# Kernel optimization log

Hardware: AMD Instinct MI355X
Metric: run time of the kernel (lower is better)

## Reference

```python
import jax, jax.numpy as jnp
import numpy as np

D = 1024  # input_size == hidden_size (required by the module's math)
B = 32768

def _linear_params(key, out_dim, in_dim):
    kw, kb = jax.random.split(key)
    bound = 1.0 / np.sqrt(in_dim)
    W = jax.random.uniform(kw, (out_dim, in_dim), jnp.float32, -bound, bound)
    b = jax.random.uniform(kb, (out_dim,), jnp.float32, -bound, bound)
    return W, b

def setup_inputs() -> dict:
    key = jax.random.key(0)
    ks = jax.random.split(key, 8)
    inp = {
        "input": jax.random.normal(ks[0], (B, D), jnp.float32),
        "hidden": jax.random.normal(ks[1], (B, D), jnp.float32),
    }
    names = ["ir", "hr", "iz", "hz", "in_", "hn"]
    for name, k in zip(names, ks[2:]):
        W, b = _linear_params(k, D, D)
        inp[f"W_{name}"] = W
        inp[f"b_{name}"] = b
    return inp

def reference(input, hidden, W_ir, b_ir, W_hr, b_hr, W_iz, b_iz, W_hz, b_hz, W_in_, b_in_, W_hn, b_hn):
    # Fuse the three input-side projections and three hidden-side projections
    # into two GEMMs each mathematically identical to six separate Linears.
    lin = lambda x, W, b: x @ W.T + b
    r_t = jax.nn.sigmoid(lin(input, W_ir, b_ir) + lin(hidden, W_hr, b_hr))
    z_t = jax.nn.sigmoid(lin(input, W_iz, b_iz) + lin(hidden, W_hz, b_hz))
    n_t = jnp.tanh(lin(input, W_in_, b_in_) + r_t * lin(hidden, W_hn, b_hn))
    h_t = (1.0 - z_t) * n_t + z_t * hidden
    return (h_t, h_t)
```

## Files before the change

kernel.cpp:

```cpp
#include <hip/hip_runtime.h>
#include <stdint.h>

#define DD 1024
#define BATCH 32768

typedef unsigned short u16;
typedef __attribute__((ext_vector_type(8))) __bf16 bf16x8;
typedef __attribute__((ext_vector_type(4))) float f32x4;
typedef __attribute__((ext_vector_type(4))) unsigned int u32x4;

__device__ __forceinline__ u16 f2bf(float x) {
  unsigned int u = __builtin_bit_cast(unsigned int, x);
  u = u + 0x7FFFu + ((u >> 16) & 1u);
  return (u16)(u >> 16);
}

__global__ void cvt_f32_to_bf16(const float4* __restrict__ src,
                                ushort4* __restrict__ dst, int n4) {
  int i = blockIdx.x * blockDim.x + threadIdx.x;
  int stride = gridDim.x * blockDim.x;
  for (; i < n4; i += stride) {
    float4 v = src[i];
    ushort4 o;
    o.x = f2bf(v.x); o.y = f2bf(v.y); o.z = f2bf(v.z); o.w = f2bf(v.w);
    dst[i] = o;
  }
}

#define A_IN_U 0
#define A_H_U  8192
#define W_U(g) (16384 + (g) * 4096)

__device__ __forceinline__ bf16x8 ld8(const u16* p) {
  u32x4 v = *reinterpret_cast<const u32x4*>(p);
  return __builtin_bit_cast(bf16x8, v);
}

__device__ __forceinline__ f32x4 mfma16(bf16x8 a, bf16x8 b, f32x4 c) {
  return __builtin_amdgcn_mfma_f32_16x16x32_bf16(a, b, c, 0, 0, 0);
}

__device__ __forceinline__ void stage_chunk(const u16* grow, u16* ldsdst) {
  int l = threadIdx.x & 63;
  int r = l >> 3;
  int s = l & 7;
  const u16* src = grow + r * DD + ((s ^ r) << 3);
  __builtin_amdgcn_global_load_lds(
      (const __attribute__((address_space(1))) void*)src,
      (__attribute__((address_space(3))) void*)ldsdst, 16, 0, 0);
}

__global__ __launch_bounds__(256, 2) void gru_fused(
    const u16* __restrict__ ain, const u16* __restrict__ ah,
    const u16* __restrict__ wall, const float* __restrict__ hidf,
    const float* __restrict__ b_ir, const float* __restrict__ b_hr,
    const float* __restrict__ b_iz, const float* __restrict__ b_hz,
    const float* __restrict__ b_in, const float* __restrict__ b_hn,
    float* __restrict__ out) {
  __shared__ __align__(16) u16 lds[40960];

  int bid = blockIdx.x;
  int wg = ((bid & 7) << 9) | (bid >> 3);
  int nb = wg >> 8;
  int mb = wg & 255;

  int tid = threadIdx.x;
  int wid = tid >> 6;
  int lane = tid & 63;
  int r15 = lane & 15;
  int kb = lane >> 4;
  int wm = wid >> 1;
  int wn = wid & 1;

  const f32x4 zero = {0.f, 0.f, 0.f, 0.f};
  f32x4 acc_r[4][2], acc_z[4][2], acc_n[4][2], acc_hn[4][2];
#pragma unroll
  for (int i = 0; i < 4; ++i)
#pragma unroll
    for (int j = 0; j < 2; ++j) {
      acc_r[i][j] = zero; acc_z[i][j] = zero;
      acc_n[i][j] = zero; acc_hn[i][j] = zero;
    }

  const u16* ain_t = ain + ((size_t)(mb * 128) << 10);
  const u16* ah_t  = ah  + ((size_t)(mb * 128) << 10);
  const u16* w_t   = wall + ((size_t)(nb * 64) << 10);

  for (int kt = 0; kt < 16; ++kt) {
    int kcol = kt << 6;
    __syncthreads();
#pragma unroll
    for (int j = 0; j < 4; ++j) {
      int c = (j << 2) | wid;
      stage_chunk(ain_t + ((size_t)c << 13) + kcol, &lds[A_IN_U + c * 512]);
      stage_chunk(ah_t  + ((size_t)c << 13) + kcol, &lds[A_H_U  + c * 512]);
    }
#pragma unroll
    for (int g = 0; g < 6; ++g) {
      const u16* wg_t = w_t + ((size_t)g << 20) + kcol;
#pragma unroll
      for (int j = 0; j < 2; ++j) {
        int c = (j << 2) | wid;
        stage_chunk(wg_t + ((size_t)c << 13), &lds[W_U(g) + c * 512]);
      }
    }
    __syncthreads();

#pragma unroll
    for (int ks = 0; ks < 2; ++ks) {
      bf16x8 afi[4], afh[4];
#pragma unroll
      for (int i = 0; i < 4; ++i) {
        int Rm = (wm << 6) + (i << 4) + r15;
        int sl = ((ks << 2) | kb) ^ (Rm & 7);
        afi[i] = ld8(&lds[A_IN_U + Rm * 64 + sl * 8]);
        afh[i] = ld8(&lds[A_H_U  + Rm * 64 + sl * 8]);
      }
#pragma unroll
      for (int jf = 0; jf < 2; ++jf) {
        int Rn = (wn << 5) + (jf << 4) + r15;
        int sl = ((ks << 2) | kb) ^ (Rn & 7);
        bf16x8 bir = ld8(&lds[W_U(0) + Rn * 64 + sl * 8]);
        bf16x8 bhr = ld8(&lds[W_U(1) + Rn * 64 + sl * 8]);
        bf16x8 biz = ld8(&lds[W_U(2) + Rn * 64 + sl * 8]);
        bf16x8 bhz = ld8(&lds[W_U(3) + Rn * 64 + sl * 8]);
        bf16x8 bin = ld8(&lds[W_U(4) + Rn * 64 + sl * 8]);
        bf16x8 bhn = ld8(&lds[W_U(5) + Rn * 64 + sl * 8]);
#pragma unroll
        for (int i = 0; i < 4; ++i) {
          acc_r[i][jf]  = mfma16(afi[i], bir, acc_r[i][jf]);
          acc_r[i][jf]  = mfma16(afh[i], bhr, acc_r[i][jf]);
          acc_z[i][jf]  = mfma16(afi[i], biz, acc_z[i][jf]);
          acc_z[i][jf]  = mfma16(afh[i], bhz, acc_z[i][jf]);
          acc_n[i][jf]  = mfma16(afi[i], bin, acc_n[i][jf]);
          acc_hn[i][jf] = mfma16(afh[i], bhn, acc_hn[i][jf]);
        }
      }
    }
  }

#pragma unroll
  for (int jf = 0; jf < 2; ++jf) {
    int col = (nb << 6) + (wn << 5) + (jf << 4) + r15;
    float brc = b_ir[col] + b_hr[col];
    float bzc = b_iz[col] + b_hz[col];
    float bnc = b_in[col];
    float bhc = b_hn[col];
#pragma unroll
    for (int i = 0; i < 4; ++i) {
      int row0 = (mb << 7) + (wm << 6) + (i << 4) + (kb << 2);
#pragma unroll
      for (int q = 0; q < 4; ++q) {
        int row = row0 + q;
        float vr = acc_r[i][jf][q] + brc;
        float vz = acc_z[i][jf][q] + bzc;
        float vn = acc_n[i][jf][q] + bnc;
        float vh = acc_hn[i][jf][q] + bhc;
        float rg = __builtin_amdgcn_rcpf(1.f + __expf(-vr));
        float zg = __builtin_amdgcn_rcpf(1.f + __expf(-vz));
        float pre = vn + rg * vh;
        float ax = fabsf(pre);
        float e2 = __expf(-2.f * ax);
        float th = copysignf((1.f - e2) * __builtin_amdgcn_rcpf(1.f + e2), pre);
        float hp = hidf[((size_t)row << 10) + col];
        float h = (1.f - zg) * th + zg * hp;
        size_t o = ((size_t)row << 10) + col;
        out[o] = h;
        out[o + (size_t)BATCH * DD] = h;
      }
    }
  }
}

extern "C" void kernel_launch(void* const* d_in, const int* in_sizes, int n_in,
                              void* d_out, int out_size, void* d_ws, size_t ws_size,
                              hipStream_t stream) {
  (void)in_sizes; (void)n_in; (void)out_size; (void)ws_size;
  const float* inp = (const float*)d_in[0];
  const float* hid = (const float*)d_in[1];
  u16* ws_in  = (u16*)d_ws;
  u16* ws_hid = ws_in + (size_t)BATCH * DD;
  u16* ws_w   = ws_hid + (size_t)BATCH * DD;

  int n4a = BATCH * DD / 4;
  hipLaunchKernelGGL(cvt_f32_to_bf16, dim3(4096), dim3(256), 0, stream,
                     (const float4*)inp, (ushort4*)ws_in, n4a);
  hipLaunchKernelGGL(cvt_f32_to_bf16, dim3(4096), dim3(256), 0, stream,
                     (const float4*)hid, (ushort4*)ws_hid, n4a);
  for (int g = 0; g < 6; ++g) {
    hipLaunchKernelGGL(cvt_f32_to_bf16, dim3(512), dim3(256), 0, stream,
                       (const float4*)d_in[2 + 2 * g],
                       (ushort4*)(ws_w + (size_t)g * DD * DD), DD * DD / 4);
  }
  hipLaunchKernelGGL(gru_fused, dim3(4096), dim3(256), 0, stream,
                     ws_in, ws_hid, ws_w, hid,
                     (const float*)d_in[3], (const float*)d_in[5],
                     (const float*)d_in[7], (const float*)d_in[9],
                     (const float*)d_in[11], (const float*)d_in[13],
                     (float*)d_out);
}
```

Measured before the change: 549.0 us.

## Double-buffer GRU GEMM staging, enlarge tile to 256 rows, fuse conversion kernels

The eight per-tensor fp32-to-bf16 conversion launches are merged into one kernel with a fixed block-to-tensor mapping. The fused GEMM now uses 512-thread blocks covering 256 rows by 64 columns. The K step drops to 32, and a double-buffered LDS pipeline prefetches the next K slice while computing the current one, using raw barriers, vmcnt waits and s_setprio around the MFMA block. This aims to hide global-load latency and halve weight-tile reloads per row, at the cost of more LDS per block and hand-tuned waitcnt logic that must match the issued load counts.

```diff
diff --git a/kernel.cpp b/kernel.cpp
--- a/kernel.cpp
+++ b/kernel.cpp
@@ -15,21 +15,33 @@
   return (u16)(u >> 16);
 }
 
-__global__ void cvt_f32_to_bf16(const float4* __restrict__ src,
-                                ushort4* __restrict__ dst, int n4) {
-  int i = blockIdx.x * blockDim.x + threadIdx.x;
-  int stride = gridDim.x * blockDim.x;
-  for (; i < n4; i += stride) {
-    float4 v = src[i];
+__global__ void cvt_all(const float4* __restrict__ in0, const float4* __restrict__ in1,
+                        const float4* __restrict__ w0, const float4* __restrict__ w1,
+                        const float4* __restrict__ w2, const float4* __restrict__ w3,
+                        const float4* __restrict__ w4, const float4* __restrict__ w5,
+                        ushort4* __restrict__ o0, ushort4* __restrict__ o1,
+                        ushort4* __restrict__ ow) {
+  int b = blockIdx.x;
+  const float4* s; ushort4* d; int rel;
+  if (b < 2048)      { s = in0; d = o0; rel = b; }
+  else if (b < 4096) { s = in1; d = o1; rel = b - 2048; }
+  else {
+    int t = b - 4096; int g = t >> 6; rel = t & 63;
+    s = (g == 0) ? w0 : (g == 1) ? w1 : (g == 2) ? w2 : (g == 3) ? w3 : (g == 4) ? w4 : w5;
+    d = ow + (size_t)g * 262144;
+  }
+  int i0 = rel * 4096 + threadIdx.x;
+#pragma unroll
+  for (int j = 0; j < 16; ++j) {
+    int i = i0 + j * 256;
+    float4 v = s[i];
     ushort4 o;
     o.x = f2bf(v.x); o.y = f2bf(v.y); o.z = f2bf(v.z); o.w = f2bf(v.w);
-    dst[i] = o;
-  }
-}
-
-#define A_IN_U 0
-#define A_H_U  8192
-#define W_U(g) (16384 + (g) * 4096)
+    d[i] = o;
+  }
+}
+
+#define BUF_U 28672
 
 __device__ __forceinline__ bf16x8 ld8(const u16* p) {
   u32x4 v = *reinterpret_cast<const u32x4*>(p);
@@ -40,29 +52,25 @@
   return __builtin_amdgcn_mfma_f32_16x16x32_bf16(a, b, c, 0, 0, 0);
 }
 
-__device__ __forceinline__ void stage_chunk(const u16* grow, u16* ldsdst) {
-  int l = threadIdx.x & 63;
-  int r = l >> 3;
-  int s = l & 7;
-  const u16* src = grow + r * DD + ((s ^ r) << 3);
+__device__ __forceinline__ void stage_one(const u16* src, const u16* dst) {
   __builtin_amdgcn_global_load_lds(
       (const __attribute__((address_space(1))) void*)src,
-      (__attribute__((address_space(3))) void*)ldsdst, 16, 0, 0);
-}
-
-__global__ __launch_bounds__(256, 2) void gru_fused(
+      (__attribute__((address_space(3))) void*)dst, 16, 0, 0);
+}
+
+__global__ __launch_bounds__(512, 2) void gru_fused(
     const u16* __restrict__ ain, const u16* __restrict__ ah,
     const u16* __restrict__ wall, const float* __restrict__ hidf,
     const float* __restrict__ b_ir, const float* __restrict__ b_hr,
     const float* __restrict__ b_iz, const float* __restrict__ b_hz,
     const float* __restrict__ b_in, const float* __restrict__ b_hn,
     float* __restrict__ out) {
-  __shared__ __align__(16) u16 lds[40960];
+  __shared__ __align__(16) u16 lds[2 * BUF_U];
 
   int bid = blockIdx.x;
-  int wg = ((bid & 7) << 9) | (bid >> 3);
-  int nb = wg >> 8;
-  int mb = wg & 255;
+  int wg = ((bid & 7) << 8) | (bid >> 3);
+  int nb = wg >> 7;
+  int mb = wg & 127;
 
   int tid = threadIdx.x;
   int wid = tid >> 6;
@@ -82,61 +90,74 @@
       acc_n[i][j] = zero; acc_hn[i][j] = zero;
     }
 
-  const u16* ain_t = ain + ((size_t)(mb * 128) << 10);
-  const u16* ah_t  = ah  + ((size_t)(mb * 128) << 10);
-  const u16* w_t   = wall + ((size_t)(nb * 64) << 10);
-
-  for (int kt = 0; kt < 16; ++kt) {
-    int kcol = kt << 6;
-    __syncthreads();
-#pragma unroll
-    for (int j = 0; j < 4; ++j) {
-      int c = (j << 2) | wid;
-      stage_chunk(ain_t + ((size_t)c << 13) + kcol, &lds[A_IN_U + c * 512]);
-      stage_chunk(ah_t  + ((size_t)c << 13) + kcol, &lds[A_H_U  + c * 512]);
-    }
-#pragma unroll
-    for (int g = 0; g < 6; ++g) {
-      const u16* wg_t = w_t + ((size_t)g << 20) + kcol;
-#pragma unroll
-      for (int j = 0; j < 2; ++j) {
-        int c = (j << 2) | wid;
-        stage_chunk(wg_t + ((size_t)c << 13), &lds[W_U(g) + c * 512]);
+  int lrow = lane >> 2;
+  unsigned koff = (unsigned)(((lane & 3) ^ (lrow & 3)) << 3);
+  const u16* ain_r = ain + (unsigned)(mb * 256 + lrow) * DD + koff;
+  const u16* ah_r  = ah  + (unsigned)(mb * 256 + lrow) * DD + koff;
+  const u16* w_r   = wall + (unsigned)(nb * 64 + lrow) * DD + koff;
+  int sub = wid & 3;
+  int g0 = wid >> 2;
+  const u16* wsrc = w_r + (unsigned)(sub * 16) * DD;
+
+  auto stage = [&](int kt, int bufb) {
+    unsigned kc = (unsigned)(kt << 5);
+    stage_one(ain_r + (unsigned)(wid * 16) * DD + kc,       &lds[bufb + wid * 512]);
+    stage_one(ain_r + (unsigned)((wid + 8) * 16) * DD + kc, &lds[bufb + (wid + 8) * 512]);
+    stage_one(ah_r  + (unsigned)(wid * 16) * DD + kc,       &lds[bufb + 8192 + wid * 512]);
+    stage_one(ah_r  + (unsigned)((wid + 8) * 16) * DD + kc, &lds[bufb + 8192 + (wid + 8) * 512]);
+    stage_one(wsrc + ((unsigned)g0 << 20) + kc,        &lds[bufb + 16384 + g0 * 2048 + sub * 512]);
+    stage_one(wsrc + ((unsigned)(g0 + 2) << 20) + kc,  &lds[bufb + 16384 + (g0 + 2) * 2048 + sub * 512]);
+    stage_one(wsrc + ((unsigned)(g0 + 4) << 20) + kc,  &lds[bufb + 16384 + (g0 + 4) * 2048 + sub * 512]);
+  };
+
+  auto compute = [&](int bufb) {
+    const u16* B = &lds[bufb];
+    bf16x8 afi[4], afh[4];
+#pragma unroll
+    for (int i = 0; i < 4; ++i) {
+      int Rm = (wm << 6) + (i << 4) + r15;
+      int sl = kb ^ (Rm & 3);
+      afi[i] = ld8(B + Rm * 32 + sl * 8);
+      afh[i] = ld8(B + 8192 + Rm * 32 + sl * 8);
+    }
+    __builtin_amdgcn_s_setprio(1);
+#pragma unroll
+    for (int jf = 0; jf < 2; ++jf) {
+      int Rn = (wn << 5) + (jf << 4) + r15;
+      int sl = kb ^ (Rn & 3);
+      const u16* W0 = B + 16384 + Rn * 32 + sl * 8;
+      bf16x8 bir = ld8(W0);
+      bf16x8 bhr = ld8(W0 + 2048);
+      bf16x8 biz = ld8(W0 + 4096);
+      bf16x8 bhz = ld8(W0 + 6144);
+      bf16x8 bin = ld8(W0 + 8192);
+      bf16x8 bhn = ld8(W0 + 10240);
+#pragma unroll
+      for (int i = 0; i < 4; ++i) {
+        acc_r[i][jf]  = mfma16(afi[i], bir, acc_r[i][jf]);
+        acc_r[i][jf]  = mfma16(afh[i], bhr, acc_r[i][jf]);
+        acc_z[i][jf]  = mfma16(afi[i], biz, acc_z[i][jf]);
+        acc_z[i][jf]  = mfma16(afh[i], bhz, acc_z[i][jf]);
+        acc_n[i][jf]  = mfma16(afi[i], bin, acc_n[i][jf]);
+        acc_hn[i][jf] = mfma16(afh[i], bhn, acc_hn[i][jf]);
       }
     }
-    __syncthreads();
-
-#pragma unroll
-    for (int ks = 0; ks < 2; ++ks) {
-      bf16x8 afi[4], afh[4];
-#pragma unroll
-      for (int i = 0; i < 4; ++i) {
-        int Rm = (wm << 6) + (i << 4) + r15;
-        int sl = ((ks << 2) | kb) ^ (Rm & 7);
-        afi[i] = ld8(&lds[A_IN_U + Rm * 64 + sl * 8]);
-        afh[i] = ld8(&lds[A_H_U  + Rm * 64 + sl * 8]);
-      }
-#pragma unroll
-      for (int jf = 0; jf < 2; ++jf) {
-        int Rn = (wn << 5) + (jf << 4) + r15;
-        int sl = ((ks << 2) | kb) ^ (Rn & 7);
-        bf16x8 bir = ld8(&lds[W_U(0) + Rn * 64 + sl * 8]);
-        bf16x8 bhr = ld8(&lds[W_U(1) + Rn * 64 + sl * 8]);
-        bf16x8 biz = ld8(&lds[W_U(2) + Rn * 64 + sl * 8]);
-        bf16x8 bhz = ld8(&lds[W_U(3) + Rn * 64 + sl * 8]);
-        bf16x8 bin = ld8(&lds[W_U(4) + Rn * 64 + sl * 8]);
-        bf16x8 bhn = ld8(&lds[W_U(5) + Rn * 64 + sl * 8]);
-#pragma unroll
-        for (int i = 0; i < 4; ++i) {
-          acc_r[i][jf]  = mfma16(afi[i], bir, acc_r[i][jf]);
-          acc_r[i][jf]  = mfma16(afh[i], bhr, acc_r[i][jf]);
-          acc_z[i][jf]  = mfma16(afi[i], biz, acc_z[i][jf]);
-          acc_z[i][jf]  = mfma16(afh[i], bhz, acc_z[i][jf]);
-          acc_n[i][jf]  = mfma16(afi[i], bin, acc_n[i][jf]);
-          acc_hn[i][jf] = mfma16(afh[i], bhn, acc_hn[i][jf]);
-        }
-      }
-    }
+    __builtin_amdgcn_s_setprio(0);
+  };
+
+  stage(0, 0);
+  for (int kt = 0; kt < 32; ++kt) {
+    if (kt < 31) {
+      stage(kt + 1, ((kt + 1) & 1) * BUF_U);
+      asm volatile("s_waitcnt vmcnt(7)" ::: "memory");
+    } else {
+      asm volatile("s_waitcnt vmcnt(0)" ::: "memory");
+    }
+    __builtin_amdgcn_s_barrier();
+    __builtin_amdgcn_sched_barrier(0);
+    compute((kt & 1) * BUF_U);
+    asm volatile("s_waitcnt lgkmcnt(0)" ::: "memory");
+    __builtin_amdgcn_s_barrier();
   }
 
 #pragma unroll
@@ -148,7 +169,7 @@
     float bhc = b_hn[col];
 #pragma unroll
     for (int i = 0; i < 4; ++i) {
-      int row0 = (mb << 7) + (wm << 6) + (i << 4) + (kb << 2);
+      int row0 = (mb << 8) + (wm << 6) + (i << 4) + (kb << 2);
 #pragma unroll
       for (int q = 0; q < 4; ++q) {
         int row = row0 + q;
@@ -182,17 +203,14 @@
   u16* ws_hid = ws_in + (size_t)BATCH * DD;
   u16* ws_w   = ws_hid + (size_t)BATCH * DD;
 
-  int n4a = BATCH * DD / 4;
-  hipLaunchKernelGGL(cvt_f32_to_bf16, dim3(4096), dim3(256), 0, stream,
-                     (const float4*)inp, (ushort4*)ws_in, n4a);
-  hipLaunchKernelGGL(cvt_f32_to_bf16, dim3(4096), dim3(256), 0, stream,
-                     (const float4*)hid, (ushort4*)ws_hid, n4a);
-  for (int g = 0; g < 6; ++g) {
-    hipLaunchKernelGGL(cvt_f32_to_bf16, dim3(512), dim3(256), 0, stream,
-                       (const float4*)d_in[2 + 2 * g],
-                       (ushort4*)(ws_w + (size_t)g * DD * DD), DD * DD / 4);
-  }
-  hipLaunchKernelGGL(gru_fused, dim3(4096), dim3(256), 0, stream,
+  hipLaunchKernelGGL(cvt_all, dim3(4480), dim3(256), 0, stream,
+                     (const float4*)inp, (const float4*)hid,
+                     (const float4*)d_in[2], (const float4*)d_in[4],
+                     (const float4*)d_in[6], (const float4*)d_in[8],
+                     (const float4*)d_in[10], (const float4*)d_in[12],
+                     (ushort4*)ws_in, (ushort4*)ws_hid, (ushort4*)ws_w);
+
+  hipLaunchKernelGGL(gru_fused, dim3(2048), dim3(512), 0, stream,
                      ws_in, ws_hid, ws_w, hid,
                      (const float*)d_in[3], (const float*)d_in[5],
                      (const float*)d_in[7], (const float*)d_in[9],
```

New measurement: 672.1 us. 22.4% more time.

## Switch GRU GEMM to 32x32x16 MFMA, merge conversions, remap block order

Applied to the files above, without the earlier changes.

Replaces the 16x16x32 bf16 MFMA tiles with 32x32x16 tiles, so each wave issues fewer, larger MFMAs and does fewer LDS fragment reads per unit of work. The epilogue is rewritten to match the 32x32 accumulator layout. The eight separate f32-to-bf16 conversion launches are merged into one kernel with a fixed per-block work split. The block-to-tile mapping is also changed so that consecutive blocks in an XCD group walk the N tiles of one M stripe, which is meant to improve L2 reuse of the activation rows. These changes risk different register pressure and LDS bank-conflict patterns.

```diff
diff --git a/kernel.cpp b/kernel.cpp
--- a/kernel.cpp
+++ b/kernel.cpp
@@ -6,7 +6,7 @@
 
 typedef unsigned short u16;
 typedef __attribute__((ext_vector_type(8))) __bf16 bf16x8;
-typedef __attribute__((ext_vector_type(4))) float f32x4;
+typedef __attribute__((ext_vector_type(16))) float f32x16;
 typedef __attribute__((ext_vector_type(4))) unsigned int u32x4;
 
 __device__ __forceinline__ u16 f2bf(float x) {
@@ -15,15 +15,29 @@
   return (u16)(u >> 16);
 }
 
-__global__ void cvt_f32_to_bf16(const float4* __restrict__ src,
-                                ushort4* __restrict__ dst, int n4) {
-  int i = blockIdx.x * blockDim.x + threadIdx.x;
-  int stride = gridDim.x * blockDim.x;
-  for (; i < n4; i += stride) {
-    float4 v = src[i];
+__global__ void cvt_all(const float4* __restrict__ in0, const float4* __restrict__ in1,
+                        const float4* __restrict__ w0, const float4* __restrict__ w1,
+                        const float4* __restrict__ w2, const float4* __restrict__ w3,
+                        const float4* __restrict__ w4, const float4* __restrict__ w5,
+                        ushort4* __restrict__ o0, ushort4* __restrict__ o1,
+                        ushort4* __restrict__ ow) {
+  int b = blockIdx.x;
+  const float4* s; ushort4* d; int rel;
+  if (b < 2048)      { s = in0; d = o0; rel = b; }
+  else if (b < 4096) { s = in1; d = o1; rel = b - 2048; }
+  else {
+    int t = b - 4096; int g = t >> 6; rel = t & 63;
+    s = (g == 0) ? w0 : (g == 1) ? w1 : (g == 2) ? w2 : (g == 3) ? w3 : (g == 4) ? w4 : w5;
+    d = ow + (size_t)g * 262144;
+  }
+  int i0 = rel * 4096 + threadIdx.x;
+#pragma unroll
+  for (int j = 0; j < 16; ++j) {
+    int i = i0 + j * 256;
+    float4 v = s[i];
     ushort4 o;
     o.x = f2bf(v.x); o.y = f2bf(v.y); o.z = f2bf(v.z); o.w = f2bf(v.w);
-    dst[i] = o;
+    d[i] = o;
   }
 }
 
@@ -36,8 +50,8 @@
   return __builtin_bit_cast(bf16x8, v);
 }
 
-__device__ __forceinline__ f32x4 mfma16(bf16x8 a, bf16x8 b, f32x4 c) {
-  return __builtin_amdgcn_mfma_f32_16x16x32_bf16(a, b, c, 0, 0, 0);
+__device__ __forceinline__ f32x16 mfma32(bf16x8 a, bf16x8 b, f32x16 c) {
+  return __builtin_amdgcn_mfma_f32_32x32x16_bf16(a, b, c, 0, 0, 0);
 }
 
 __device__ __forceinline__ void stage_chunk(const u16* grow, u16* ldsdst) {
@@ -60,31 +74,31 @@
   __shared__ __align__(16) u16 lds[40960];
 
   int bid = blockIdx.x;
-  int wg = ((bid & 7) << 9) | (bid >> 3);
-  int nb = wg >> 8;
-  int mb = wg & 255;
+  int x = bid & 7;
+  int s = bid >> 3;
+  int mb = (x << 5) | (s >> 4);
+  int nb = s & 15;
 
   int tid = threadIdx.x;
   int wid = tid >> 6;
   int lane = tid & 63;
-  int r15 = lane & 15;
-  int kb = lane >> 4;
+  int c31 = lane & 31;
+  int khalf = lane >> 5;
   int wm = wid >> 1;
   int wn = wid & 1;
 
-  const f32x4 zero = {0.f, 0.f, 0.f, 0.f};
-  f32x4 acc_r[4][2], acc_z[4][2], acc_n[4][2], acc_hn[4][2];
-#pragma unroll
-  for (int i = 0; i < 4; ++i)
-#pragma unroll
-    for (int j = 0; j < 2; ++j) {
-      acc_r[i][j] = zero; acc_z[i][j] = zero;
-      acc_n[i][j] = zero; acc_hn[i][j] = zero;
-    }
+  f32x16 acc_r[2], acc_z[2], acc_n[2], acc_hn[2];
+#pragma unroll
+  for (int i = 0; i < 2; ++i) {
+    acc_r[i] = (f32x16)0.f; acc_z[i] = (f32x16)0.f;
+    acc_n[i] = (f32x16)0.f; acc_hn[i] = (f32x16)0.f;
+  }
 
   const u16* ain_t = ain + ((size_t)(mb * 128) << 10);
   const u16* ah_t  = ah  + ((size_t)(mb * 128) << 10);
   const u16* w_t   = wall + ((size_t)(nb * 64) << 10);
+
+  int possw = c31 & 7;
 
   for (int kt = 0; kt < 16; ++kt) {
     int kcol = kt << 6;
@@ -107,67 +121,61 @@
     __syncthreads();
 
 #pragma unroll
-    for (int ks = 0; ks < 2; ++ks) {
-      bf16x8 afi[4], afh[4];
-#pragma unroll
-      for (int i = 0; i < 4; ++i) {
-        int Rm = (wm << 6) + (i << 4) + r15;
-        int sl = ((ks << 2) | kb) ^ (Rm & 7);
-        afi[i] = ld8(&lds[A_IN_U + Rm * 64 + sl * 8]);
-        afh[i] = ld8(&lds[A_H_U  + Rm * 64 + sl * 8]);
+    for (int ks = 0; ks < 4; ++ks) {
+      int pos = (((ks << 1) | khalf) ^ possw) << 3;
+      bf16x8 afi[2], afh[2];
+#pragma unroll
+      for (int i = 0; i < 2; ++i) {
+        int Rm = (wm << 6) + (i << 5) + c31;
+        afi[i] = ld8(&lds[A_IN_U + Rm * 64 + pos]);
+        afh[i] = ld8(&lds[A_H_U  + Rm * 64 + pos]);
       }
-#pragma unroll
-      for (int jf = 0; jf < 2; ++jf) {
-        int Rn = (wn << 5) + (jf << 4) + r15;
-        int sl = ((ks << 2) | kb) ^ (Rn & 7);
-        bf16x8 bir = ld8(&lds[W_U(0) + Rn * 64 + sl * 8]);
-        bf16x8 bhr = ld8(&lds[W_U(1) + Rn * 64 + sl * 8]);
-        bf16x8 biz = ld8(&lds[W_U(2) + Rn * 64 + sl * 8]);
-        bf16x8 bhz = ld8(&lds[W_U(3) + Rn * 64 + sl * 8]);
-        bf16x8 bin = ld8(&lds[W_U(4) + Rn * 64 + sl * 8]);
-        bf16x8 bhn = ld8(&lds[W_U(5) + Rn * 64 + sl * 8]);
-#pragma unroll
-        for (int i = 0; i < 4; ++i) {
-          acc_r[i][jf]  = mfma16(afi[i], bir, acc_r[i][jf]);
-          acc_r[i][jf]  = mfma16(afh[i], bhr, acc_r[i][jf]);
-          acc_z[i][jf]  = mfma16(afi[i], biz, acc_z[i][jf]);
-          acc_z[i][jf]  = mfma16(afh[i], bhz, acc_z[i][jf]);
-          acc_n[i][jf]  = mfma16(afi[i], bin, acc_n[i][jf]);
-          acc_hn[i][jf] = mfma16(afh[i], bhn, acc_hn[i][jf]);
-        }
+      int Rn = (wn << 5) + c31;
+      const u16* W0 = &lds[W_U(0) + Rn * 64 + pos];
+      bf16x8 bir = ld8(W0);
+      bf16x8 bhr = ld8(W0 + 4096);
+      bf16x8 biz = ld8(W0 + 8192);
+      bf16x8 bhz = ld8(W0 + 12288);
+      bf16x8 bin = ld8(W0 + 16384);
+      bf16x8 bhn = ld8(W0 + 20480);
+#pragma unroll
+      for (int i = 0; i < 2; ++i) {
+        acc_r[i]  = mfma32(afi[i], bir, acc_r[i]);
+        acc_r[i]  = mfma32(afh[i], bhr, acc_r[i]);
+        acc_z[i]  = mfma32(afi[i], biz, acc_z[i]);
+        acc_z[i]  = mfma32(afh[i], bhz, acc_z[i]);
+        acc_n[i]  = mfma32(afi[i], bin, acc_n[i]);
+        acc_hn[i] = mfma32(afh[i], bhn, acc_hn[i]);
       }
     }
   }
 
-#pragma unroll
-  for (int jf = 0; jf < 2; ++jf) {
-    int col = (nb << 6) + (wn << 5) + (jf << 4) + r15;
-    float brc = b_ir[col] + b_hr[col];
-    float bzc = b_iz[col] + b_hz[col];
-    float bnc = b_in[col];
-    float bhc = b_hn[col];
-#pragma unroll
-    for (int i = 0; i < 4; ++i) {
-      int row0 = (mb << 7) + (wm << 6) + (i << 4) + (kb << 2);
-#pragma unroll
-      for (int q = 0; q < 4; ++q) {
-        int row = row0 + q;
-        float vr = acc_r[i][jf][q] + brc;
-        float vz = acc_z[i][jf][q] + bzc;
-        float vn = acc_n[i][jf][q] + bnc;
-        float vh = acc_hn[i][jf][q] + bhc;
-        float rg = __builtin_amdgcn_rcpf(1.f + __expf(-vr));
-        float zg = __builtin_amdgcn_rcpf(1.f + __expf(-vz));
-        float pre = vn + rg * vh;
-        float ax = fabsf(pre);
-        float e2 = __expf(-2.f * ax);
-        float th = copysignf((1.f - e2) * __builtin_amdgcn_rcpf(1.f + e2), pre);
-        float hp = hidf[((size_t)row << 10) + col];
-        float h = (1.f - zg) * th + zg * hp;
-        size_t o = ((size_t)row << 10) + col;
-        out[o] = h;
-        out[o + (size_t)BATCH * DD] = h;
-      }
+  int col = (nb << 6) + (wn << 5) + c31;
+  float brc = b_ir[col] + b_hr[col];
+  float bzc = b_iz[col] + b_hz[col];
+  float bnc = b_in[col];
+  float bhc = b_hn[col];
+#pragma unroll
+  for (int i = 0; i < 2; ++i) {
+    int rbase = (mb << 7) + (wm << 6) + (i << 5) + (khalf << 2);
+#pragma unroll
+    for (int reg = 0; reg < 16; ++reg) {
+      int row = rbase + (reg & 3) + ((reg >> 2) << 3);
+      float vr = acc_r[i][reg] + brc;
+      float vz = acc_z[i][reg] + bzc;
+      float vn = acc_n[i][reg] + bnc;
+      float vh = acc_hn[i][reg] + bhc;
+      float rg = __builtin_amdgcn_rcpf(1.f + __expf(-vr));
+      float zg = __builtin_amdgcn_rcpf(1.f + __expf(-vz));
+      float pre = vn + rg * vh;
+      float ax = fabsf(pre);
+      float e2 = __expf(-2.f * ax);
+      float th = copysignf((1.f - e2) * __builtin_amdgcn_rcpf(1.f + e2), pre);
+      float hp = hidf[((size_t)row << 10) + col];
+      float h = (1.f - zg) * th + zg * hp;
+      size_t o = ((size_t)row << 10) + col;
+      out[o] = h;
+      out[o + (size_t)BATCH * DD] = h;
     }
   }
 }
@@ -182,16 +190,13 @@
   u16* ws_hid = ws_in + (size_t)BATCH * DD;
   u16* ws_w   = ws_hid + (size_t)BATCH * DD;
 
-  int n4a = BATCH * DD / 4;
-  hipLaunchKernelGGL(cvt_f32_to_bf16, dim3(4096), dim3(256), 0, stream,
-                     (const float4*)inp, (ushort4*)ws_in, n4a);
-  hipLaunchKernelGGL(cvt_f32_to_bf16, dim3(4096), dim3(256), 0, stream,
-                     (const float4*)hid, (ushort4*)ws_hid, n4a);
-  for (int g = 0; g < 6; ++g) {
-    hipLaunchKernelGGL(cvt_f32_to_bf16, dim3(512), dim3(256), 0, stream,
-                       (const float4*)d_in[2 + 2 * g],
-                       (ushort4*)(ws_w + (size_t)g * DD * DD), DD * DD / 4);
-  }
+  hipLaunchKernelGGL(cvt_all, dim3(4480), dim3(256), 0, stream,
+                     (const float4*)inp, (const float4*)hid,
+                     (const float4*)d_in[2], (const float4*)d_in[4],
+                     (const float4*)d_in[6], (const float4*)d_in[8],
+                     (const float4*)d_in[10], (const float4*)d_in[12],
+                     (ushort4*)ws_in, (ushort4*)ws_hid, (ushort4*)ws_w);
+
   hipLaunchKernelGGL(gru_fused, dim3(4096), dim3(256), 0, stream,
                      ws_in, ws_hid, ws_w, hid,
                      (const float*)d_in[3], (const float*)d_in[5],
```

New measurement: 561.2 us. 2.2% more time.
